# Kernel optimization log

Hardware: AMD Instinct MI355X
Metric: run time of the kernel (lower is better)

The kernel has to match this reference:

```python
import jax, jax.numpy as jnp
import numpy as np
from jax import lax

SR = 4      # sr_ratio
HEADS = 8   # num_heads


def _upsample_bilinear_ac(x, out_h, out_w):
    # torch nn.Upsample(scale_factor=SR, mode='bilinear', align_corners=True)
    B, C, h, w = x.shape
    ys = jnp.linspace(0.0, h - 1.0, out_h)
    xs = jnp.linspace(0.0, w - 1.0, out_w)
    y0 = jnp.floor(ys).astype(jnp.int32)
    y1 = jnp.minimum(y0 + 1, h - 1)
    wy = (ys - y0).astype(x.dtype)
    x0 = jnp.floor(xs).astype(jnp.int32)
    x1 = jnp.minimum(x0 + 1, w - 1)
    wx = (xs - x0).astype(x.dtype)
    r = x[:, :, y0, :] * (1.0 - wy)[None, None, :, None] + x[:, :, y1, :] * wy[None, None, :, None]
    return r[:, :, :, x0] * (1.0 - wx) + r[:, :, :, x1] * wx


def _forward(x, sr_w, sr_b, ln_g, ln_b, q_w, k1_w, v1_w, k2_w, v2_w, proj_w, proj_b):
    B, C, H, W = x.shape
    ID = C // 4                      # internal_dim
    hd = ID // HEADS                 # head_dim
    scale = float(hd) ** -0.5
    # spatial-reduction conv for Q path: [B, ID, H/4, W/4]
    qf = lax.conv_general_dilated(x, sr_w, (SR, SR), 'VALID',
                                  dimension_numbers=('NCHW', 'OIHW', 'NCHW'))
    qf = qf + sr_b[None, :, None, None]
    Hs, Ws = qf.shape[2], qf.shape[3]
    N = Hs * Ws
    qf = qf.reshape(B, ID, N).transpose(0, 2, 1)          # [B, N, ID]
    # LayerNorm
    mu = qf.mean(-1, keepdims=True)
    var = qf.var(-1, keepdims=True)
    qn = (qf - mu) / jnp.sqrt(var + 1e-5) * ln_g + ln_b
    q = qn @ q_w                                          # [B, N, ID]
    # max / avg pooled K,V inputs: [B, N, C]
    xm = lax.reduce_window(x, -jnp.inf, lax.max, (1, 1, SR, SR), (1, 1, SR, SR), 'VALID')
    xm = xm.reshape(B, C, N).transpose(0, 2, 1)
    xa = lax.reduce_window(x, 0.0, lax.add, (1, 1, SR, SR), (1, 1, SR, SR), 'VALID') / float(SR * SR)
    xa = xa.reshape(B, C, N).transpose(0, 2, 1)

    def heads(t):
        return t.reshape(B, N, HEADS, hd).transpose(0, 2, 1, 3)  # [B, H, N, hd]

    qh = heads(q)
    k1, v1 = heads(xm @ k1_w), heads(xm @ v1_w)
    k2, v2 = heads(xa @ k2_w), heads(xa @ v2_w)

    def attend(k, v):
        a = jax.nn.softmax(jnp.einsum('bhnd,bhmd->bhnm', qh, k) * scale, axis=-1)
        return jnp.einsum('bhnm,bhmd->bhnd', a, v)

    z = attend(k1, v1) + attend(k2, v2)                   # [B, H, N, hd]
    z = z.transpose(0, 2, 1, 3).reshape(B, N, ID)
    z = z @ proj_w + proj_b                               # [B, N, C]
    z = z.transpose(0, 2, 1).reshape(B, C, Hs, Ws)
    return _upsample_bilinear_ac(z, H, W)


def setup_inputs() -> dict:
    key = jax.random.key(0)
    ks = jax.random.split(key, 9)
    B, C, H, W = 16, 256, 112, 112
    ID = C // 4

    def n(k, shape, s=0.02):
        return jax.random.normal(k, shape, jnp.float32) * s

    return {
        'x': jax.random.normal(ks[0], (B, C, H, W), jnp.float32),
        'sr_w': n(ks[1], (ID, C, SR, SR)),
        'sr_b': jnp.zeros((ID,), jnp.float32),
        'ln_g': jnp.ones((ID,), jnp.float32),
        'ln_b': jnp.zeros((ID,), jnp.float32),
        'q_w': n(ks[2], (ID, ID)),
        'k1_w': n(ks[3], (C, ID)),
        'v1_w': n(ks[4], (C, ID)),
        'k2_w': n(ks[5], (C, ID)),
        'v2_w': n(ks[6], (C, ID)),
        'proj_w': n(ks[7], (ID, C)),
        'proj_b': jnp.zeros((C,), jnp.float32),
    }


def reference(x, sr_w, sr_b, ln_g, ln_b, q_w, k1_w, v1_w, k2_w, v2_w, proj_w, proj_b):
    return _forward(x, sr_w, sr_b, ln_g, ln_b, q_w, k1_w, v1_w, k2_w, v2_w, proj_w, proj_b)
```

## Files before the change

### kernel.cpp

```cpp
#include <hip/hip_runtime.h>
#include <math.h>

typedef __attribute__((ext_vector_type(8))) short short8;
typedef __attribute__((ext_vector_type(4))) short bh4;
typedef __attribute__((ext_vector_type(4))) float f32x4;
typedef __attribute__((ext_vector_type(2))) unsigned uint2v;
typedef __attribute__((ext_vector_type(4))) unsigned uint4v;

#define MFMA16(A,B,C) __builtin_amdgcn_mfma_f32_16x16x32_bf16(A,B,C,0,0,0)

#if __has_builtin(__builtin_amdgcn_mfma_f32_16x16x16bf16_1k)
#define MFMA16x16(A,B,C) __builtin_amdgcn_mfma_f32_16x16x16bf16_1k(A,B,C,0,0,0)
#else
__device__ __forceinline__ f32x4 mfma16x16_asm(bh4 a, bh4 b, f32x4 c){
    asm volatile("v_mfma_f32_16x16x16_bf16 %0, %1, %2, %0" : "+v"(c) : "v"(a), "v"(b));
    return c;
}
#define MFMA16x16(A,B,C) mfma16x16_asm(A,B,C)
#endif

__device__ __forceinline__ unsigned short f2b(float f){
    unsigned u = __builtin_bit_cast(unsigned, f);
    return (unsigned short)((u + 0x7fffu + ((u>>16)&1u)) >> 16);
}
__device__ __forceinline__ unsigned pk2(float a, float b){
    return (unsigned)f2b(a) | ((unsigned)f2b(b) << 16);
}
__device__ __forceinline__ unsigned pk2rn(float a, float b){
    unsigned ua = __builtin_bit_cast(unsigned, a) + 0x8000u;
    unsigned ub = __builtin_bit_cast(unsigned, b) + 0x8000u;
    return (ua >> 16) | (ub & 0xffff0000u);
}


__global__ __launch_bounds__(256) void ktw(const float* __restrict__ srw,
    const float* __restrict__ qw, const float* __restrict__ k1w,
    const float* __restrict__ v1w, const float* __restrict__ k2w,
    const float* __restrict__ v2w, char* __restrict__ srwb,
    char* __restrict__ Wtm, char* __restrict__ Wta, char* __restrict__ QWt)
{
    int blk = blockIdx.x, t = threadIdx.x;
    if (blk < 128){
        int base = blk*2048 + t*8;
        float4 a = *(const float4*)(srw + base);
        float4 b = *(const float4*)(srw + base + 4);
        uint4 u = { pk2(a.x,a.y), pk2(a.z,a.w), pk2(b.x,b.y), pk2(b.z,b.w) };
        *(uint4*)(srwb + (size_t)base*2) = u;
    } else if (blk < 136){
        __shared__ float T[256*33];
        int idx = blk - 128, fi = idx >> 1, half = idx & 1;
        const float* src = (fi==0) ? k1w : (fi==1) ? v1w : (fi==2) ? k2w : v2w;
        char* dst = ((fi < 2) ? Wtm : Wta) + (size_t)((fi & 1)*64 + half*32) * 512;
        for (int li = t; li < 8192; li += 256){
            int c = li >> 5, o = li & 31;
            T[c*33 + o] = src[c*64 + half*32 + o];
        }
        __syncthreads();
        for (int lo = t; lo < 1024; lo += 256){
            int o = lo >> 5, c8 = lo & 31;
            float v[8];
            #pragma unroll
            for (int k = 0; k < 8; ++k) v[k] = T[(c8*8 + k)*33 + o];
            uint4 u = { pk2(v[0],v[1]), pk2(v[2],v[3]), pk2(v[4],v[5]), pk2(v[6],v[7]) };
            *(uint4*)(dst + o*512 + c8*16) = u;
        }
    } else {
        __shared__ float T[64*65];
        for (int li = t; li < 4096; li += 256)
            T[(li >> 6)*65 + (li & 63)] = qw[li];
        __syncthreads();
        for (int lo = t; lo < 512; lo += 256){
            int o = lo >> 3, i8 = lo & 7;
            float v[8];
            #pragma unroll
            for (int k = 0; k < 8; ++k) v[k] = T[(i8*8 + k)*65 + o];
            uint4 u = { pk2(v[0],v[1]), pk2(v[2],v[3]), pk2(v[4],v[5]), pk2(v[6],v[7]) };
            *(uint4*)(QWt + o*128 + i8*16) = u;
        }
    }
}

__global__ __launch_bounds__(256, 4) void k1(const float* __restrict__ x,
    const char* __restrict__ srwb, char* __restrict__ R, float* __restrict__ pws)
{
    __shared__ float pm[28*66];
    __shared__ float pa[28*66];
    int blk = blockIdx.x;
    int b = blk / 112, r5 = blk % 112, hs = r5 >> 2, cg4 = r5 & 3;
    int t = threadIdx.x;
    int w = t >> 6, l = t & 63, lr = l & 15, lg = l >> 4;
    int cpar = lg >> 1, r0 = (lg & 1) * 2;
    f32x4 acc0 = {0.f,0.f,0.f,0.f}, acc1 = {0.f,0.f,0.f,0.f};
    const float* xc = x + (size_t)(b*256 + cg4*64)*12544 + (size_t)(hs*4 + r0)*112;
    const char* Brow = srwb + (size_t)(w*16 + lr)*8192 + cg4*2048 + lg*16;
    int p0 = lr, p1 = min(16 + lr, 27);
    size_t rowB = (size_t)b*784 + hs*28;

    float4 XA0,XA1,XA2,XA3,XA4,XA5,XA6,XA7; short8 BA0,BA1;
    float4 XB0,XB1,XB2,XB3,XB4,XB5,XB6,XB7; short8 BB0,BB1;

#define LD2(X0,X1,X2,X3,X4,X5,X6,X7,Bq0,Bq1,KS) do{ \
    const float* _s0 = xc + (size_t)((KS)*2 + cpar)*12544; \
    const float* _s1 = xc + (size_t)(((KS)+1)*2 + cpar)*12544; \
    X0=*(const float4*)(_s0+p0*4); X1=*(const float4*)(_s0+112+p0*4); \
    X2=*(const float4*)(_s0+p1*4); X3=*(const float4*)(_s0+112+p1*4); \
    X4=*(const float4*)(_s1+p0*4); X5=*(const float4*)(_s1+112+p0*4); \
    X6=*(const float4*)(_s1+p1*4); X7=*(const float4*)(_s1+112+p1*4); \
    Bq0=*(const short8*)(Brow+(KS)*64); Bq1=*(const short8*)(Brow+((KS)+1)*64); }while(0)

#define PROC1(Y0,Y1,Y2,Y3,BF,KS) do{ \
    if (w == 0){ \
        float mx0 = fmaxf(fmaxf(fmaxf(Y0.x,Y0.y),fmaxf(Y0.z,Y0.w)), \
                          fmaxf(fmaxf(Y1.x,Y1.y),fmaxf(Y1.z,Y1.w))); \
        float sm0 = (Y0.x+Y0.y)+(Y0.z+Y0.w)+(Y1.x+Y1.y)+(Y1.z+Y1.w); \
        float mx1 = fmaxf(fmaxf(fmaxf(Y2.x,Y2.y),fmaxf(Y2.z,Y2.w)), \
                          fmaxf(fmaxf(Y3.x,Y3.y),fmaxf(Y3.z,Y3.w))); \
        float sm1 = (Y2.x+Y2.y)+(Y2.z+Y2.w)+(Y3.x+Y3.y)+(Y3.z+Y3.w); \
        mx0 = fmaxf(mx0, __shfl_xor(mx0, 16, 64)); \
        sm0 = sm0 + __shfl_xor(sm0, 16, 64); \
        mx1 = fmaxf(mx1, __shfl_xor(mx1, 16, 64)); \
        sm1 = sm1 + __shfl_xor(sm1, 16, 64); \
        if ((lg & 1) == 0){ \
            int c = (KS)*2 + cpar; \
            pm[p0*66 + c] = mx0; pa[p0*66 + c] = sm0 * (1.f/16.f); \
            if (lr < 12){ pm[p1*66 + c] = mx1; pa[p1*66 + c] = sm1 * (1.f/16.f); } \
        } \
    } \
    short8 af0 = __builtin_bit_cast(short8, \
        (uint4v){ pk2(Y0.x,Y0.y), pk2(Y0.z,Y0.w), pk2(Y1.x,Y1.y), pk2(Y1.z,Y1.w) }); \
    short8 af1 = __builtin_bit_cast(short8, \
        (uint4v){ pk2(Y2.x,Y2.y), pk2(Y2.z,Y2.w), pk2(Y3.x,Y3.y), pk2(Y3.z,Y3.w) }); \
    acc0 = MFMA16(af0, BF, acc0); \
    acc1 = MFMA16(af1, BF, acc1); }while(0)

    LD2(XA0,XA1,XA2,XA3,XA4,XA5,XA6,XA7,BA0,BA1, 0);
    #pragma unroll
    for (int s2 = 0; s2 < 8; ++s2){
        int ka = s2*4;
        LD2(XB0,XB1,XB2,XB3,XB4,XB5,XB6,XB7,BB0,BB1, ka+2);
        PROC1(XA0,XA1,XA2,XA3,BA0, ka);
        PROC1(XA4,XA5,XA6,XA7,BA1, ka+1);
        if (s2 < 7) LD2(XA0,XA1,XA2,XA3,XA4,XA5,XA6,XA7,BA0,BA1, ka+4);
        PROC1(XB0,XB1,XB2,XB3,BB0, ka+2);
        PROC1(XB4,XB5,XB6,XB7,BB1, ka+3);
    }
#undef LD2
#undef PROC1

    float* pp = pws + (size_t)((b*28 + hs)*4 + cg4)*1792;
    #pragma unroll
    for (int rg = 0; rg < 4; ++rg){
        int m0 = lg*4 + rg, m1 = 16 + lg*4 + rg;
        pp[m0*64 + w*16 + lr] = acc0[rg];
        if (m1 < 28) pp[m1*64 + w*16 + lr] = acc1[rg];
    }
    __syncthreads();
    if (t < 224){
        int m = t >> 3, sub = t & 7;
        float vm[8], va8[8];
        #pragma unroll
        for (int k = 0; k < 8; ++k){
            vm[k]  = pm[m*66 + sub*8 + k];
            va8[k] = pa[m*66 + sub*8 + k];
        }
        uint4 um = { pk2(vm[0],vm[1]), pk2(vm[2],vm[3]), pk2(vm[4],vm[5]), pk2(vm[6],vm[7]) };
        uint4 ua = { pk2(va8[0],va8[1]), pk2(va8[2],va8[3]), pk2(va8[4],va8[5]), pk2(va8[6],va8[7]) };
        *(uint4*)(R + (rowB + m)*1024 + cg4*128 + sub*16)       = um;
        *(uint4*)(R + (rowB + m)*1024 + 512 + cg4*128 + sub*16) = ua;
    }
}

__global__ __launch_bounds__(512) void k2(const float* __restrict__ pws_,
    const float* __restrict__ srb, const float* __restrict__ lng,
    const float* __restrict__ lnb, const char* __restrict__ Wtm,
    const char* __restrict__ Wta, const char* __restrict__ QWt,
    char* __restrict__ R)
{
    __shared__ __align__(16) char PM[16384];
    __shared__ __align__(16) char PA[16384];
    __shared__ float Db[32*64];
    __shared__ __align__(16) char QN[4096];
    int blk = blockIdx.x, b = blk/28, hs = blk%28;
    int t = threadIdx.x, w = t>>6, l = t&63, lr = l&15, lg = l>>4;
    size_t rowB = (size_t)b*784 + hs*28;
    const char* Rb = R + rowB*1024;
    for (int li = t; li < 896; li += 512){
        int m = li >> 5, c16 = li & 31;
        uint4 vm = *(const uint4*)(Rb + (size_t)m*1024 + c16*16);
        uint4 va = *(const uint4*)(Rb + (size_t)m*1024 + 512 + c16*16);
        int dst = m*512 + ((c16*16) ^ ((m&7)<<4));
        *(uint4*)(PM + dst) = vm;
        *(uint4*)(PA + dst) = va;
    }
    const float* p0 = pws_ + (size_t)(b*28 + hs)*4*1792;
    for (int e = t; e < 1792; e += 512)
        Db[e] = ((p0[e] + p0[1792+e]) + (p0[3584+e] + p0[5376+e])) + srb[e & 63];
    __syncthreads();
    float g = lng[l], be = lnb[l];
    #pragma unroll
    for (int i = 0; i < 4; ++i){
        int m = w + i*8;
        float v = Db[m*64 + l];
        float s = v, ss = v*v;
        #pragma unroll
        for (int off = 1; off < 64; off <<= 1){
            s  += __shfl_xor(s,  off, 64);
            ss += __shfl_xor(ss, off, 64);
        }
        float mu = s * (1.f/64.f);
        float var = ss * (1.f/64.f) - mu*mu;
        float qn = (v - mu) * rsqrtf(var + 1e-5f) * g + be;
        *(unsigned short*)(QN + m*128 + ((l*2) ^ ((m&7)<<4))) = f2b(qn);
    }
    __syncthreads();
    int fam = w >> 2, ofp = w & 3;
    const char* PMA = fam ? PA : PM;
    const char* Wt  = fam ? Wta : Wtm;
    f32x4 a00={0.f,0.f,0.f,0.f}, a01=a00, a10=a00, a11=a00;
    int swzr = (lr & 7) << 4;
    #pragma unroll
    for (int ks = 0; ks < 8; ++ks){
        int kb = ks*64 + lg*16;
        short8 x0 = *(const short8*)(PMA + lr*512 + (kb ^ swzr));
        short8 x1 = *(const short8*)(PMA + (16+lr)*512 + (kb ^ swzr));
        short8 b0 = *(const short8*)(Wt + (size_t)(ofp*32 + lr)*512 + kb);
        short8 b1 = *(const short8*)(Wt + (size_t)(ofp*32 + 16 + lr)*512 + kb);
        a00 = MFMA16(x0, b0, a00); a01 = MFMA16(x0, b1, a01);
        a10 = MFMA16(x1, b0, a10); a11 = MFMA16(x1, b1, a11);
    }
    f32x4 q0={0.f,0.f,0.f,0.f}, q1=q0;
    if (w < 4){
        #pragma unroll
        for (int ks = 0; ks < 2; ++ks){
            int kb = ks*64 + lg*16;
            short8 xa_ = *(const short8*)(QN + lr*128 + (kb ^ swzr));
            short8 xb_ = *(const short8*)(QN + (16+lr)*128 + (kb ^ swzr));
            short8 bq  = *(const short8*)(QWt + (size_t)(w*16 + lr)*128 + kb);
            q0 = MFMA16(xa_, bq, q0);
            q1 = MFMA16(xb_, bq, q1);
        }
    }
    #pragma unroll
    for (int j = 0; j < 2; ++j){
        int o128 = ofp*32 + j*16 + lr;
        int o = o128 & 63, hh = o >> 3, dd = o & 7, mat = fam*2 + (o128 >> 6);
        int byteoff = 128 + hh*64 + mat*16 + dd*2;
        f32x4 am  = j ? a01 : a00;
        f32x4 am1 = j ? a11 : a10;
        #pragma unroll
        for (int rg = 0; rg < 4; ++rg){
            int m0 = lg*4 + rg, m1 = 16 + lg*4 + rg;
            *(unsigned short*)(R + (rowB + m0)*1024 + byteoff) = f2b(am[rg]);
            if (m1 < 28)
                *(unsigned short*)(R + (rowB + m1)*1024 + byteoff) = f2b(am1[rg]);
        }
    }
    if (w < 4){
        int o = w*16 + lr;
        #pragma unroll
        for (int rg = 0; rg < 4; ++rg){
            int m0 = lg*4 + rg, m1 = 16 + lg*4 + rg;
            *(unsigned short*)(R + (rowB + m0)*1024 + o*2) = f2b(q0[rg]);
            if (m1 < 28)
                *(unsigned short*)(R + (rowB + m1)*1024 + o*2) = f2b(q1[rg]);
        }
    }
}

__global__ __launch_bounds__(256) void kattn(const char* __restrict__ R, float* __restrict__ z)
{
    __shared__ __align__(16) char QT [6144];
    __shared__ __align__(16) char K1b[5376];
    __shared__ __align__(16) char K2b[5376];
    __shared__ __align__(16) char VT1[3840];
    __shared__ __align__(16) char VT2[3840];
    int blk = blockIdx.x;
    int bh = blk / 7, nseg = blk % 7;
    int b = bh >> 3, h = bh & 7;
    int t = threadIdx.x, w = t >> 6, l = t & 63;
    int col = l & 15, g = l >> 4;

    for (int i = t; i < 384; i += 256) ((uint4*)QT)[i] = uint4{0,0,0,0};
    for (int i = t; i < 112; i += 256){
        *(uint4*)(K1b + i*48 + 16) = uint4{0,0,0,0};
        *(uint4*)(K2b + i*48 + 16) = uint4{0,0,0,0};
    }
    for (int i = t; i < 120; i += 256){
        *(uint4*)(VT1 + 1920 + i*16) = uint4{0,0,0,0};
        *(uint4*)(VT2 + 1920 + i*16) = uint4{0,0,0,0};
    }
    __syncthreads();
    if (t < 112){
        uint4 qv = *(const uint4*)(R + ((size_t)b*784 + nseg*112 + t)*1024 + h*16);
        *(uint2*)(QT + t*48)     = uint2{qv.x, qv.y};
        *(uint2*)(QT + t*48 + 8) = uint2{qv.z, qv.w};
    }
    __syncthreads();

    bh4 qf[2];
    #pragma unroll
    for (int nf = 0; nf < 2; ++nf)
        qf[nf] = *(const bh4*)(QT + (w*28 + nf*16 + col)*48 + g*8);

    f32x4 o1[2] = {{0,0,0,0},{0,0,0,0}}, o2[2] = {{0,0,0,0},{0,0,0,0}};
    float d1[2] = {0.f,0.f}, d2[2] = {0.f,0.f};
    const float C2 = 0.51004244f;

    for (int mt = 0; mt < 7; ++mt){
        __syncthreads();
        for (int li = t; li < 448; li += 256){
            int m = li >> 2, part = li & 3;
            uint4 v = *(const uint4*)(R + ((size_t)b*784 + mt*112 + m)*1024 + 128 + h*64 + part*16);
            if ((part & 1) == 0){
                char* Kb = (part == 0) ? K1b : K2b;
                *(uint2*)(Kb + m*48)     = uint2{v.x, v.y};
                *(uint2*)(Kb + m*48 + 8) = uint2{v.z, v.w};
            } else {
                char* Vb = (part == 1) ? VT1 : VT2;
                unsigned arr[4] = {v.x, v.y, v.z, v.w};
                #pragma unroll
                for (int d = 0; d < 4; ++d){
                    *(unsigned short*)(Vb + (d*2)*240   + m*2) = (unsigned short)(arr[d] & 0xffffu);
                    *(unsigned short*)(Vb + (d*2+1)*240 + m*2) = (unsigned short)(arr[d] >> 16);
                }
            }
        }
        __syncthreads();
        #pragma unroll
        for (int mc = 0; mc < 7; ++mc){
            bh4 ka = *(const bh4*)(K1b + (mc*16 + col)*48 + g*8);
            bh4 kb = *(const bh4*)(K2b + (mc*16 + col)*48 + g*8);
            bh4 va = *(const bh4*)(VT1 + col*240 + mc*32 + g*8);
            bh4 vb = *(const bh4*)(VT2 + col*240 + mc*32 + g*8);
            #pragma unroll
            for (int nf = 0; nf < 2; ++nf){
                f32x4 zr = {0.f,0.f,0.f,0.f};
                f32x4 s1 = MFMA16x16(ka, qf[nf], zr);
                float p0 = exp2f(s1[0]*C2), p1 = exp2f(s1[1]*C2);
                float p2 = exp2f(s1[2]*C2), p3 = exp2f(s1[3]*C2);
                d1[nf] += (p0+p1)+(p2+p3);
                bh4 pf1 = __builtin_bit_cast(bh4, (uint2v){pk2rn(p0,p1), pk2rn(p2,p3)});
                o1[nf] = MFMA16x16(va, pf1, o1[nf]);
                f32x4 s2 = MFMA16x16(kb, qf[nf], zr);
                float r0 = exp2f(s2[0]*C2), r1 = exp2f(s2[1]*C2);
                float r2 = exp2f(s2[2]*C2), r3 = exp2f(s2[3]*C2);
                d2[nf] += (r0+r1)+(r2+r3);
                bh4 pf2 = __builtin_bit_cast(bh4, (uint2v){pk2rn(r0,r1), pk2rn(r2,r3)});
                o2[nf] = MFMA16x16(vb, pf2, o2[nf]);
            }
        }
    }
    #pragma unroll
    for (int nf = 0; nf < 2; ++nf){
        d1[nf] += __shfl_xor(d1[nf], 16, 64); d1[nf] += __shfl_xor(d1[nf], 32, 64);
        d2[nf] += __shfl_xor(d2[nf], 16, 64); d2[nf] += __shfl_xor(d2[nf], 32, 64);
    }
    if (g < 2){
        #pragma unroll
        for (int nf = 0; nf < 2; ++nf){
            if (nf == 1 && col >= 12) continue;
            int n = nseg*112 + w*28 + nf*16 + col;
            float ra = 1.f / d1[nf], rb = 1.f / d2[nf];
            float4 ov;
            ov.x = o1[nf][0]*ra + o2[nf][0]*rb;
            ov.y = o1[nf][1]*ra + o2[nf][1]*rb;
            ov.z = o1[nf][2]*ra + o2[nf][2]*rb;
            ov.w = o1[nf][3]*ra + o2[nf][3]*rb;
            *(float4*)(z + ((size_t)b*784 + n)*64 + h*8 + g*4) = ov;
        }
    }
}

__global__ __launch_bounds__(256) void kpu(const float* __restrict__ z,
    const float* __restrict__ pw, const float* __restrict__ pb,
    float* __restrict__ out)
{
    __shared__ float plane[8*784];
    __shared__ float wsl[64*8];
    __shared__ int   ti0[112];
    __shared__ float twv[112];
    int blk = blockIdx.x;
    int b = blk >> 5, cg = blk & 31;
    int t = threadIdx.x;
    if (t < 128){
        #pragma unroll
        for (int q = 0; q < 4; ++q){
            int idx = t*4 + q; int o = idx >> 3, j = idx & 7;
            wsl[o*8 + j] = pw[o*256 + cg*8 + j];
        }
    }
    if (t < 112){
        float s = (float)t * (27.f/111.f);
        int i0 = (int)s; if (i0 > 27) i0 = 27;
        ti0[t] = i0; twv[t] = s - (float)i0;
    }
    __syncthreads();
    {
        int nh = t >> 1, jh = (t & 1) * 4;
        float bias0 = pb[cg*8 + jh], bias1 = pb[cg*8 + jh + 1];
        float bias2 = pb[cg*8 + jh + 2], bias3 = pb[cg*8 + jh + 3];
        for (int n = nh; n < 784; n += 128){
            const float* zr = z + ((size_t)b*784 + n)*64;
            float a0 = bias0, a1 = bias1, a2 = bias2, a3 = bias3;
            #pragma unroll
            for (int o4 = 0; o4 < 16; ++o4){
                float4 zv = *(const float4*)(zr + o4*4);
                const float* wr = wsl + (o4*4)*8 + jh;
                a0 = fmaf(zv.x, wr[0],  a0); a1 = fmaf(zv.x, wr[1],  a1);
                a2 = fmaf(zv.x, wr[2],  a2); a3 = fmaf(zv.x, wr[3],  a3);
                a0 = fmaf(zv.y, wr[8],  a0); a1 = fmaf(zv.y, wr[9],  a1);
                a2 = fmaf(zv.y, wr[10], a2); a3 = fmaf(zv.y, wr[11], a3);
                a0 = fmaf(zv.z, wr[16], a0); a1 = fmaf(zv.z, wr[17], a1);
                a2 = fmaf(zv.z, wr[18], a2); a3 = fmaf(zv.z, wr[19], a3);
                a0 = fmaf(zv.w, wr[24], a0); a1 = fmaf(zv.w, wr[25], a1);
                a2 = fmaf(zv.w, wr[26], a2); a3 = fmaf(zv.w, wr[27], a3);
            }
            plane[(jh+0)*784 + n] = a0;
            plane[(jh+1)*784 + n] = a1;
            plane[(jh+2)*784 + n] = a2;
            plane[(jh+3)*784 + n] = a3;
        }
    }
    __syncthreads();
    float* ob = out + ((size_t)b*256 + cg*8)*12544;
    for (int i = t; i < 12544; i += 256){
        int y = i/112, xx = i%112;
        int y0 = ti0[y], x0 = ti0[xx];
        float wy = twv[y], wx = twv[xx];
        int y1 = min(y0+1, 27), x1 = min(x0+1, 27);
        int i00 = y0*28 + x0, i01 = y0*28 + x1, i10 = y1*28 + x0, i11 = y1*28 + x1;
        #pragma unroll
        for (int j = 0; j < 8; ++j){
            const float* pl = plane + j*784;
            float a  = pl[i00] + (pl[i10]-pl[i00])*wy;
            float bb = pl[i01] + (pl[i11]-pl[i01])*wy;
            ob[(size_t)j*12544 + i] = a + (bb-a)*wx;
        }
    }
}

extern "C" void kernel_launch(void* const* d_in, const int* in_sizes, int n_in,
                              void* d_out, int out_size, void* d_ws, size_t ws_size,
                              hipStream_t stream) {
    const float* x   = (const float*)d_in[0];
    const float* srw = (const float*)d_in[1];
    const float* srb = (const float*)d_in[2];
    const float* lng = (const float*)d_in[3];
    const float* lnb = (const float*)d_in[4];
    const float* qw  = (const float*)d_in[5];
    const float* k1w = (const float*)d_in[6];
    const float* v1w = (const float*)d_in[7];
    const float* k2w = (const float*)d_in[8];
    const float* v2w = (const float*)d_in[9];
    const float* pw  = (const float*)d_in[10];
    const float* pb  = (const float*)d_in[11];

    char*  Rws  = (char*)d_ws;
    float* pws  = (float*)(Rws + 12845056);
    char*  srwb = Rws + 25690112;
    char*  Wtm  = Rws + 26214400;
    char*  Wta  = Rws + 26279936;
    char*  QWt  = Rws + 26345472;
    float* z    = (float*)(Rws + 12845056);
    float* out  = (float*)d_out;

    ktw  <<<137,  256, 0, stream>>>(srw, qw, k1w, v1w, k2w, v2w, srwb, Wtm, Wta, QWt);
    k1   <<<1792, 256, 0, stream>>>(x, srwb, Rws, pws);
    k2   <<<448,  512, 0, stream>>>(pws, srb, lng, lnb, Wtm, Wta, QWt, Rws);
    kattn<<<896,  256, 0, stream>>>(Rws, z);
    kpu  <<<512,  256, 0, stream>>>(z, pw, pb, out);
}
```

Measured before the change: 258.2 us.

## Stage k1 input tiles into LDS via async global_load_lds double buffering

Kernel k1 (stride-4 conv plus max/avg pooling) now copies each 8-channel slab of x into shared memory with direct global-to-LDS loads, double-buffered across two LDS buffers with explicit vmcnt waits and barriers. The MFMA A-fragments and the pooling reductions are then read from LDS, and the pooling is spread over 224 threads instead of wave 0 only. Max and avg are packed as one bf16 pair per LDS slot. The aim is to overlap HBM streaming with compute and to remove the shuffle-heavy single-wave pooling. In exchange it uses about 28KB of extra LDS, drops the occupancy hint of 4 blocks, and adds barriers per stage.

```diff
diff --git a/kernel.cpp b/kernel.cpp
--- a/kernel.cpp
+++ b/kernel.cpp
@@ -30,6 +30,11 @@
     unsigned ua = __builtin_bit_cast(unsigned, a) + 0x8000u;
     unsigned ub = __builtin_bit_cast(unsigned, b) + 0x8000u;
     return (ua >> 16) | (ub & 0xffff0000u);
+}
+__device__ __forceinline__ void gl_lds16(const void* g, void* l){
+    __builtin_amdgcn_global_load_lds(
+        (const __attribute__((address_space(1))) void*)g,
+        (__attribute__((address_space(3))) void*)l, 16, 0, 0);
 }
 
 
@@ -80,73 +85,106 @@
     }
 }
 
-__global__ __launch_bounds__(256, 4) void k1(const float* __restrict__ x,
+__global__ __launch_bounds__(256) void k1(const float* __restrict__ x,
     const char* __restrict__ srwb, char* __restrict__ R, float* __restrict__ pws)
 {
-    __shared__ float pm[28*66];
-    __shared__ float pa[28*66];
+    __shared__ __align__(16) char Xb0[14336];
+    __shared__ __align__(16) char Xb1[14336];
+    __shared__ unsigned pmpa[28*66];
     int blk = blockIdx.x;
     int b = blk / 112, r5 = blk % 112, hs = r5 >> 2, cg4 = r5 & 3;
     int t = threadIdx.x;
     int w = t >> 6, l = t & 63, lr = l & 15, lg = l >> 4;
-    int cpar = lg >> 1, r0 = (lg & 1) * 2;
+    int p0 = lr, p1m = min(16 + lr, 27);
+    int nIss = (w < 3) ? 4 : 2;
+    int jbase = (w < 3) ? w*4 : 12;
+
+    size_t gchunk[4]; int ldso[4];
+    #pragma unroll
+    for (int q = 0; q < 4; ++q){
+        int byte_in = (jbase + q)*1024 + l*16;
+        int c = byte_in / 1792, rem = byte_in - c*1792;
+        gchunk[q] = (size_t)c*50176 + rem;
+        ldso[q] = (jbase + q)*1024;
+    }
+    const char* xstage = (const char*)x
+        + ((size_t)(b*256 + cg4*64)*12544 + (size_t)hs*448)*4;
+    const char* bRow = srwb + (size_t)(w*16 + lr)*8192 + cg4*2048 + lg*16;
+    int pl_p = t >> 3, pl_c = t & 7;
+
     f32x4 acc0 = {0.f,0.f,0.f,0.f}, acc1 = {0.f,0.f,0.f,0.f};
-    const float* xc = x + (size_t)(b*256 + cg4*64)*12544 + (size_t)(hs*4 + r0)*112;
-    const char* Brow = srwb + (size_t)(w*16 + lr)*8192 + cg4*2048 + lg*16;
-    int p0 = lr, p1 = min(16 + lr, 27);
+    short8 bfA0,bfA1,bfA2,bfA3, bfB0,bfB1,bfB2,bfB3;
+
+#define BPRE(B0,B1,B2,B3,S) do{ \
+    B0 = *(const short8*)(bRow + (S)*256);      \
+    B1 = *(const short8*)(bRow + (S)*256 + 64); \
+    B2 = *(const short8*)(bRow + (S)*256 + 128);\
+    B3 = *(const short8*)(bRow + (S)*256 + 192); }while(0)
+
+#define STAGE(XB,S) do{ \
+    const char* _gb = xstage + (size_t)(S)*401408; \
+    _Pragma("unroll") for (int q = 0; q < 4; ++q){ \
+        if (q < nIss) gl_lds16(_gb + gchunk[q], XB + ldso[q]); } }while(0)
+
+#define WAITP do{ if (w < 3) asm volatile("s_waitcnt vmcnt(8)" ::: "memory"); \
+                  else       asm volatile("s_waitcnt vmcnt(6)" ::: "memory"); }while(0)
+#define WAIT0 asm volatile("s_waitcnt vmcnt(0)" ::: "memory")
+#define BAR   do{ __builtin_amdgcn_s_barrier(); __builtin_amdgcn_sched_barrier(0); }while(0)
+
+#define COMP(XB,B0,B1,B2,B3,S) do{ \
+    if (t < 224){ \
+        const char* cb = XB + pl_c*1792 + pl_p*16; \
+        f32x4 r0 = *(const f32x4*)(cb);        f32x4 r1 = *(const f32x4*)(cb + 448); \
+        f32x4 r2 = *(const f32x4*)(cb + 896);  f32x4 r3 = *(const f32x4*)(cb + 1344); \
+        float mx = fmaxf(fmaxf(fmaxf(r0[0],r0[1]),fmaxf(r0[2],r0[3])), \
+                         fmaxf(fmaxf(r1[0],r1[1]),fmaxf(r1[2],r1[3]))); \
+        mx = fmaxf(mx, fmaxf(fmaxf(fmaxf(r2[0],r2[1]),fmaxf(r2[2],r2[3])), \
+                             fmaxf(fmaxf(r3[0],r3[1]),fmaxf(r3[2],r3[3])))); \
+        float sm = ((r0[0]+r0[1])+(r0[2]+r0[3])) + ((r1[0]+r1[1])+(r1[2]+r1[3])) \
+                 + ((r2[0]+r2[1])+(r2[2]+r2[3])) + ((r3[0]+r3[1])+(r3[2]+r3[3])); \
+        pmpa[pl_p*66 + (S)*8 + pl_c] = pk2(mx, sm * (1.f/16.f)); \
+    } \
+    _Pragma("unroll") for (int ks = 0; ks < 4; ++ks){ \
+        const char* abase = XB + (ks*2 + (lg>>1))*1792 + (lg&1)*896; \
+        f32x4 lo0 = *(const f32x4*)(abase + p0*16); \
+        f32x4 hi0 = *(const f32x4*)(abase + 448 + p0*16); \
+        f32x4 lo1 = *(const f32x4*)(abase + p1m*16); \
+        f32x4 hi1 = *(const f32x4*)(abase + 448 + p1m*16); \
+        short8 af0 = __builtin_bit_cast(short8, \
+            (uint4v){ pk2(lo0[0],lo0[1]), pk2(lo0[2],lo0[3]), pk2(hi0[0],hi0[1]), pk2(hi0[2],hi0[3]) }); \
+        short8 af1 = __builtin_bit_cast(short8, \
+            (uint4v){ pk2(lo1[0],lo1[1]), pk2(lo1[2],lo1[3]), pk2(hi1[0],hi1[1]), pk2(hi1[2],hi1[3]) }); \
+        short8 bq = (ks==0)?B0:(ks==1)?B1:(ks==2)?B2:B3; \
+        acc0 = MFMA16(af0, bq, acc0); \
+        acc1 = MFMA16(af1, bq, acc1); } }while(0)
+
+    BPRE(bfA0,bfA1,bfA2,bfA3, 0); STAGE(Xb0, 0);
+
+    BPRE(bfB0,bfB1,bfB2,bfB3, 1); STAGE(Xb1, 1); WAITP; BAR;
+    COMP(Xb0, bfA0,bfA1,bfA2,bfA3, 0); BAR;
+    BPRE(bfA0,bfA1,bfA2,bfA3, 2); STAGE(Xb0, 2); WAITP; BAR;
+    COMP(Xb1, bfB0,bfB1,bfB2,bfB3, 1); BAR;
+    BPRE(bfB0,bfB1,bfB2,bfB3, 3); STAGE(Xb1, 3); WAITP; BAR;
+    COMP(Xb0, bfA0,bfA1,bfA2,bfA3, 2); BAR;
+    BPRE(bfA0,bfA1,bfA2,bfA3, 4); STAGE(Xb0, 4); WAITP; BAR;
+    COMP(Xb1, bfB0,bfB1,bfB2,bfB3, 3); BAR;
+    BPRE(bfB0,bfB1,bfB2,bfB3, 5); STAGE(Xb1, 5); WAITP; BAR;
+    COMP(Xb0, bfA0,bfA1,bfA2,bfA3, 4); BAR;
+    BPRE(bfA0,bfA1,bfA2,bfA3, 6); STAGE(Xb0, 6); WAITP; BAR;
+    COMP(Xb1, bfB0,bfB1,bfB2,bfB3, 5); BAR;
+    BPRE(bfB0,bfB1,bfB2,bfB3, 7); STAGE(Xb1, 7); WAITP; BAR;
+    COMP(Xb0, bfA0,bfA1,bfA2,bfA3, 6); BAR;
+    WAIT0; BAR;
+    COMP(Xb1, bfB0,bfB1,bfB2,bfB3, 7);
+
+#undef BPRE
+#undef STAGE
+#undef WAITP
+#undef WAIT0
+#undef BAR
+#undef COMP
+
     size_t rowB = (size_t)b*784 + hs*28;
-
-    float4 XA0,XA1,XA2,XA3,XA4,XA5,XA6,XA7; short8 BA0,BA1;
-    float4 XB0,XB1,XB2,XB3,XB4,XB5,XB6,XB7; short8 BB0,BB1;
-
-#define LD2(X0,X1,X2,X3,X4,X5,X6,X7,Bq0,Bq1,KS) do{ \
-    const float* _s0 = xc + (size_t)((KS)*2 + cpar)*12544; \
-    const float* _s1 = xc + (size_t)(((KS)+1)*2 + cpar)*12544; \
-    X0=*(const float4*)(_s0+p0*4); X1=*(const float4*)(_s0+112+p0*4); \
-    X2=*(const float4*)(_s0+p1*4); X3=*(const float4*)(_s0+112+p1*4); \
-    X4=*(const float4*)(_s1+p0*4); X5=*(const float4*)(_s1+112+p0*4); \
-    X6=*(const float4*)(_s1+p1*4); X7=*(const float4*)(_s1+112+p1*4); \
-    Bq0=*(const short8*)(Brow+(KS)*64); Bq1=*(const short8*)(Brow+((KS)+1)*64); }while(0)
-
-#define PROC1(Y0,Y1,Y2,Y3,BF,KS) do{ \
-    if (w == 0){ \
-        float mx0 = fmaxf(fmaxf(fmaxf(Y0.x,Y0.y),fmaxf(Y0.z,Y0.w)), \
-                          fmaxf(fmaxf(Y1.x,Y1.y),fmaxf(Y1.z,Y1.w))); \
-        float sm0 = (Y0.x+Y0.y)+(Y0.z+Y0.w)+(Y1.x+Y1.y)+(Y1.z+Y1.w); \
-        float mx1 = fmaxf(fmaxf(fmaxf(Y2.x,Y2.y),fmaxf(Y2.z,Y2.w)), \
-                          fmaxf(fmaxf(Y3.x,Y3.y),fmaxf(Y3.z,Y3.w))); \
-        float sm1 = (Y2.x+Y2.y)+(Y2.z+Y2.w)+(Y3.x+Y3.y)+(Y3.z+Y3.w); \
-        mx0 = fmaxf(mx0, __shfl_xor(mx0, 16, 64)); \
-        sm0 = sm0 + __shfl_xor(sm0, 16, 64); \
-        mx1 = fmaxf(mx1, __shfl_xor(mx1, 16, 64)); \
-        sm1 = sm1 + __shfl_xor(sm1, 16, 64); \
-        if ((lg & 1) == 0){ \
-            int c = (KS)*2 + cpar; \
-            pm[p0*66 + c] = mx0; pa[p0*66 + c] = sm0 * (1.f/16.f); \
-            if (lr < 12){ pm[p1*66 + c] = mx1; pa[p1*66 + c] = sm1 * (1.f/16.f); } \
-        } \
-    } \
-    short8 af0 = __builtin_bit_cast(short8, \
-        (uint4v){ pk2(Y0.x,Y0.y), pk2(Y0.z,Y0.w), pk2(Y1.x,Y1.y), pk2(Y1.z,Y1.w) }); \
-    short8 af1 = __builtin_bit_cast(short8, \
-        (uint4v){ pk2(Y2.x,Y2.y), pk2(Y2.z,Y2.w), pk2(Y3.x,Y3.y), pk2(Y3.z,Y3.w) }); \
-    acc0 = MFMA16(af0, BF, acc0); \
-    acc1 = MFMA16(af1, BF, acc1); }while(0)
-
-    LD2(XA0,XA1,XA2,XA3,XA4,XA5,XA6,XA7,BA0,BA1, 0);
-    #pragma unroll
-    for (int s2 = 0; s2 < 8; ++s2){
-        int ka = s2*4;
-        LD2(XB0,XB1,XB2,XB3,XB4,XB5,XB6,XB7,BB0,BB1, ka+2);
-        PROC1(XA0,XA1,XA2,XA3,BA0, ka);
-        PROC1(XA4,XA5,XA6,XA7,BA1, ka+1);
-        if (s2 < 7) LD2(XA0,XA1,XA2,XA3,XA4,XA5,XA6,XA7,BA0,BA1, ka+4);
-        PROC1(XB0,XB1,XB2,XB3,BB0, ka+2);
-        PROC1(XB4,XB5,XB6,XB7,BB1, ka+3);
-    }
-#undef LD2
-#undef PROC1
-
     float* pp = pws + (size_t)((b*28 + hs)*4 + cg4)*1792;
     #pragma unroll
     for (int rg = 0; rg < 4; ++rg){
@@ -157,14 +195,13 @@
     __syncthreads();
     if (t < 224){
         int m = t >> 3, sub = t & 7;
-        float vm[8], va8[8];
-        #pragma unroll
-        for (int k = 0; k < 8; ++k){
-            vm[k]  = pm[m*66 + sub*8 + k];
-            va8[k] = pa[m*66 + sub*8 + k];
-        }
-        uint4 um = { pk2(vm[0],vm[1]), pk2(vm[2],vm[3]), pk2(vm[4],vm[5]), pk2(vm[6],vm[7]) };
-        uint4 ua = { pk2(va8[0],va8[1]), pk2(va8[2],va8[3]), pk2(va8[4],va8[5]), pk2(va8[6],va8[7]) };
+        unsigned u[8];
+        #pragma unroll
+        for (int k = 0; k < 8; ++k) u[k] = pmpa[m*66 + sub*8 + k];
+        uint4 um = { (u[0]&0xffffu)|(u[1]<<16), (u[2]&0xffffu)|(u[3]<<16),
+                     (u[4]&0xffffu)|(u[5]<<16), (u[6]&0xffffu)|(u[7]<<16) };
+        uint4 ua = { (u[0]>>16)|(u[1]&0xffff0000u), (u[2]>>16)|(u[3]&0xffff0000u),
+                     (u[4]>>16)|(u[5]&0xffff0000u), (u[6]>>16)|(u[7]&0xffff0000u) };
         *(uint4*)(R + (rowB + m)*1024 + cg4*128 + sub*16)       = um;
         *(uint4*)(R + (rowB + m)*1024 + 512 + cg4*128 + sub*16) = ua;
     }
```

Measured after the change: 237.0 us. 8.2% less time.
